# Kernel optimization log

Hardware: AMD Instinct MI355X
Metric: run time of the kernel (lower is better)

Reference implementation:

```python
import jax, jax.numpy as jnp
import numpy as np

TEMPERATURE = 0.9  # DiversityLoss temperature
EPS = 1e-6


def setup_inputs() -> dict:
    key = jax.random.key(0)
    kx, ke = jax.random.split(key)
    x = jax.random.normal(kx, (8, 4096, 128), dtype=jnp.float32)
    embed = jax.random.normal(ke, (2048, 128), dtype=jnp.float32)  # [codebook_size, dim]
    return {"x": x, "embed": embed}


def reference(x, embed):
    """EuclideanCodebook.forward (ema_update=True, eval mode: no buffer updates).

    Returns (quantize, embed_ind, diversity_loss).
    """
    shape = x.shape
    xf = x.reshape(-1, shape[-1])                       # [N, d]
    x_sq = jnp.sum(xf * xf, axis=1, keepdims=True)      # [N, 1]
    e_sq = jnp.sum(embed * embed, axis=1)[None, :]      # [1, K]
    confidence = -(x_sq - 2.0 * (xf @ embed.T) + e_sq)  # [N, K]
    embed_ind_flat = jnp.argmax(confidence, axis=-1)    # [N]
    # dequantize: gather codebook rows, restore leading shape
    quantize = jnp.take(embed, embed_ind_flat, axis=0).reshape(shape)
    embed_ind = embed_ind_flat.reshape(shape[:-1])
    # diversity loss: softmax over codes per point, mean over points, entropy-style sum
    point_probs = jax.nn.softmax(confidence / TEMPERATURE, axis=1)  # [N, K]
    class_probs = jnp.mean(point_probs, axis=0)                      # [K]
    diversity_loss = jnp.sum(class_probs * jnp.log(class_probs + EPS))
    return quantize, embed_ind, diversity_loss
```

## Files before the change

### kernel.cpp

```cpp
#include <hip/hip_runtime.h>
#include <math.h>

#define D        128
#define TM       64
#define TKC      64
#define ESTRIDE  136
#define INV_T    (1.0f / 0.9f)
#define LO_SCALE 4096.0f
#define LO_INV   (1.0f / 4096.0f)

typedef _Float16 half8 __attribute__((ext_vector_type(8)));
typedef float    f32x4 __attribute__((ext_vector_type(4)));

__global__ void prep_kernel(const float* __restrict__ embed,
                            float* __restrict__ e_sq,
                            _Float16* __restrict__ e_hi,
                            _Float16* __restrict__ e_lo,
                            float* __restrict__ classacc) {
    const int c = blockIdx.x;
    const int t = threadIdx.x;
    float v0 = embed[(size_t)c * D + t];
    float v1 = embed[(size_t)c * D + 64 + t];
    _Float16 h0 = (_Float16)v0;
    _Float16 h1 = (_Float16)v1;
    e_hi[(size_t)c * D + t]      = h0;
    e_hi[(size_t)c * D + 64 + t] = h1;
    e_lo[(size_t)c * D + t]      = (_Float16)((v0 - (float)h0) * LO_SCALE);
    e_lo[(size_t)c * D + 64 + t] = (_Float16)((v1 - (float)h1) * LO_SCALE);
    float s = v0 * v0 + v1 * v1;
    #pragma unroll
    for (int off = 32; off > 0; off >>= 1) s += __shfl_down(s, off, 64);
    if (t == 0) {
        e_sq[c] = s;
        classacc[c] = 0.0f;
    }
}

__device__ __forceinline__ void stage_e(const uint4* __restrict__ ehi_g4,
                                        const uint4* __restrict__ elo_g4,
                                        _Float16* ehi, _Float16* elo,
                                        int ch, int tid) {
    #pragma unroll
    for (int it = 0; it < 4; ++it) {
        int j   = tid + it * 256;
        int row = j >> 4;
        int c8  = j & 15;
        uint4 vh = ehi_g4[(size_t)ch * (TKC * 16) + j];
        uint4 vl = elo_g4[(size_t)ch * (TKC * 16) + j];
        *(uint4*)&ehi[row * ESTRIDE + c8 * 8] = vh;
        *(uint4*)&elo[row * ESTRIDE + c8 * 8] = vl;
    }
}

__device__ __forceinline__ void mfma_chunk(const _Float16* ehi, const _Float16* elo,
                                           const half8* ahi, const half8* alo,
                                           int col, int quad,
                                           f32x4 chh[4], f32x4 cx[4]) {
    #pragma unroll
    for (int kk = 0; kk < 4; ++kk) {
        #pragma unroll
        for (int t = 0; t < 4; ++t) {
            const int boff = (16 * t + col) * ESTRIDE + kk * 32 + quad * 8;
            half8 bhi = *(const half8*)&ehi[boff];
            half8 blo = *(const half8*)&elo[boff];
            chh[t] = __builtin_amdgcn_mfma_f32_16x16x32_f16(ahi[kk], bhi, chh[t], 0, 0, 0);
            cx[t]  = __builtin_amdgcn_mfma_f32_16x16x32_f16(ahi[kk], blo, cx[t], 0, 0, 0);
            cx[t]  = __builtin_amdgcn_mfma_f32_16x16x32_f16(alo[kk], bhi, cx[t], 0, 0, 0);
        }
    }
}

__global__ __launch_bounds__(256)
void fused_kernel(const float* __restrict__ x, const float* __restrict__ embed,
                  const _Float16* __restrict__ e_hi_g, const _Float16* __restrict__ e_lo_g,
                  const float* __restrict__ e_sq_g,
                  float* __restrict__ classacc,
                  float* __restrict__ q_out, float* __restrict__ ind_out, int K) {
    __shared__ _Float16 ehi[TKC * ESTRIDE];
    __shared__ _Float16 elo[TKC * ESTRIDE];
    __shared__ float esq_s[2048];
    __shared__ float cacc_s[2048];
    __shared__ float r_s[TM];
    __shared__ int   idx_s[TM];

    const int tid  = threadIdx.x;
    const int w    = tid >> 6;
    const int lane = tid & 63;
    const int col  = lane & 15;
    const int quad = lane >> 4;
    const int p0   = blockIdx.x * TM;
    const int pr   = p0 + 16 * w + col;

    for (int i = tid; i < K; i += 256) { esq_s[i] = e_sq_g[i]; cacc_s[i] = 0.0f; }

    half8 ahi[4], alo[4];
    #pragma unroll
    for (int kk = 0; kk < 4; ++kk) {
        const float* src = x + (size_t)pr * D + kk * 32 + quad * 8;
        #pragma unroll
        for (int j = 0; j < 8; ++j) {
            float v = src[j];
            _Float16 h = (_Float16)v;
            ahi[kk][j] = h;
            alo[kk][j] = (_Float16)((v - (float)h) * LO_SCALE);
        }
    }

    const uint4* ehi_g4 = (const uint4*)e_hi_g;
    const uint4* elo_g4 = (const uint4*)e_lo_g;
    const int nch = K / TKC;

    float lrun[4] = {0.f, 0.f, 0.f, 0.f};
    float bval[4] = {-INFINITY, -INFINITY, -INFINITY, -INFINITY};
    int   bidx[4] = {0, 0, 0, 0};

    for (int ch = 0; ch < nch; ++ch) {
        __syncthreads();
        stage_e(ehi_g4, elo_g4, ehi, elo, ch, tid);
        __syncthreads();
        f32x4 chh[4], cx[4];
        #pragma unroll
        for (int t = 0; t < 4; ++t) { chh[t] = (f32x4){0,0,0,0}; cx[t] = (f32x4){0,0,0,0}; }
        mfma_chunk(ehi, elo, ahi, alo, col, quad, chh, cx);
        #pragma unroll
        for (int t = 0; t < 4; ++t) {
            const int code = ch * TKC + 16 * t + col;
            const float esq = esq_s[code];
            #pragma unroll
            for (int r = 0; r < 4; ++r) {
                float s = 2.0f * (chh[t][r] + cx[t][r] * LO_INV) - esq;
                lrun[r] += __expf(s * INV_T);
                if (s > bval[r]) { bval[r] = s; bidx[r] = code; }
            }
        }
    }

    #pragma unroll
    for (int r = 0; r < 4; ++r) {
        float v = bval[r]; int bi = bidx[r]; float l = lrun[r];
        #pragma unroll
        for (int off = 8; off >= 1; off >>= 1) {
            float ov = __shfl_xor(v, off, 16);
            int   oi = __shfl_xor(bi, off, 16);
            float ol = __shfl_xor(l, off, 16);
            l += ol;
            if (ov > v || (ov == v && oi < bi)) { v = ov; bi = oi; }
        }
        if (col == 0) {
            int row = 16 * w + quad * 4 + r;
            r_s[row]   = 1.0f / l;
            idx_s[row] = bi;
            ind_out[p0 + row] = (float)bi;
        }
    }
    __syncthreads();

    float rrow[4];
    #pragma unroll
    for (int r = 0; r < 4; ++r) rrow[r] = r_s[16 * w + quad * 4 + r];

    for (int ch = 0; ch < nch; ++ch) {
        __syncthreads();
        stage_e(ehi_g4, elo_g4, ehi, elo, ch, tid);
        __syncthreads();
        f32x4 chh[4], cx[4];
        #pragma unroll
        for (int t = 0; t < 4; ++t) { chh[t] = (f32x4){0,0,0,0}; cx[t] = (f32x4){0,0,0,0}; }
        mfma_chunk(ehi, elo, ahi, alo, col, quad, chh, cx);
        #pragma unroll
        for (int t = 0; t < 4; ++t) {
            const int code = ch * TKC + 16 * t + col;
            const float esq = esq_s[code];
            float wsum = 0.0f;
            #pragma unroll
            for (int r = 0; r < 4; ++r) {
                float s = 2.0f * (chh[t][r] + cx[t][r] * LO_INV) - esq;
                wsum += __expf(s * INV_T) * rrow[r];
            }
            wsum += __shfl_xor(wsum, 16, 64);
            wsum += __shfl_xor(wsum, 32, 64);
            if (quad == 0) atomicAdd(&cacc_s[code], wsum);
        }
    }

    __syncthreads();
    for (int i = tid; i < K; i += 256) atomicAdd(&classacc[i], cacc_s[i]);

    const float4* emb4 = (const float4*)embed;
    float4* q4 = (float4*)q_out;
    #pragma unroll
    for (int it = 0; it < 8; ++it) {
        int j = tid + it * 256;
        int row = j >> 5, d4 = j & 31;
        q4[(size_t)(p0 + row) * 32 + d4] = emb4[(size_t)idx_s[row] * 32 + d4];
    }
}

__global__ void finalize_kernel(const float* __restrict__ classacc,
                                float* __restrict__ loss_out, int N, int K) {
    __shared__ float red[256];
    const int tid = threadIdx.x;
    float s = 0.0f;
    const float invN = 1.0f / (float)N;
    for (int i = tid; i < K; i += 256) {
        float cp = classacc[i] * invN;
        s += cp * logf(cp + 1e-6f);
    }
    red[tid] = s;
    __syncthreads();
    for (int off = 128; off > 0; off >>= 1) {
        if (tid < off) red[tid] += red[tid + off];
        __syncthreads();
    }
    if (tid == 0) loss_out[0] = red[0];
}

extern "C" void kernel_launch(void* const* d_in, const int* in_sizes, int n_in,
                              void* d_out, int out_size, void* d_ws, size_t ws_size,
                              hipStream_t stream) {
    const float* x     = (const float*)d_in[0];
    const float* embed = (const float*)d_in[1];
    const int N = in_sizes[0] / D;
    const int K = in_sizes[1] / D;

    float* out      = (float*)d_out;
    float* q_out    = out;
    float* ind_out  = out + (size_t)N * D;
    float* loss_out = ind_out + N;

    float*    e_sq = (float*)d_ws;
    float*    cacc = e_sq + K;
    _Float16* e_hi = (_Float16*)(cacc + K);
    _Float16* e_lo = e_hi + (size_t)K * D;

    prep_kernel<<<K, 64, 0, stream>>>(embed, e_sq, e_hi, e_lo, cacc);
    fused_kernel<<<N / TM, 256, 0, stream>>>(x, embed, e_hi, e_lo, e_sq,
                                             cacc, q_out, ind_out, K);
    finalize_kernel<<<1, 256, 0, stream>>>(cacc, loss_out, N, K);
}
```

Before: 225.7 us.

## Keep codebook slice in registers and split codes across blocks with partial combine

Replaces the single fused kernel with two sweeps. Each block keeps a 256-code codebook slice resident in registers and streams 64-point tiles of x through shared memory. A combine kernel merges per-slice max, argmax and sum-exp, and a separate gather kernel writes the quantized rows. This removes the repeated per-chunk codebook restaging through LDS and raises parallelism. In exchange it adds launches, intermediate global buffers, and converts x to hi/lo eight times per pass. Sizes are hardcoded to the test shape.

```diff
diff --git a/kernel.cpp b/kernel.cpp
--- a/kernel.cpp
+++ b/kernel.cpp
@@ -2,14 +2,19 @@
 #include <math.h>
 
 #define D        128
-#define TM       64
-#define TKC      64
-#define ESTRIDE  136
+#define KCODES   2048
+#define NPTS     32768
+#define AS       136
 #define INV_T    (1.0f / 0.9f)
 #define LO_SCALE 4096.0f
 #define LO_INV   (1.0f / 4096.0f)
+#define CHUNK    64
+#define NCHUNK   8
+#define PSLICES  64
+#define CSLICES  8
 
 typedef _Float16 half8 __attribute__((ext_vector_type(8)));
+typedef _Float16 half4 __attribute__((ext_vector_type(4)));
 typedef float    f32x4 __attribute__((ext_vector_type(4)));
 
 __global__ void prep_kernel(const float* __restrict__ embed,
@@ -36,164 +41,249 @@
     }
 }
 
-__device__ __forceinline__ void stage_e(const uint4* __restrict__ ehi_g4,
-                                        const uint4* __restrict__ elo_g4,
-                                        _Float16* ehi, _Float16* elo,
-                                        int ch, int tid) {
-    #pragma unroll
-    for (int it = 0; it < 4; ++it) {
-        int j   = tid + it * 256;
-        int row = j >> 4;
-        int c8  = j & 15;
-        uint4 vh = ehi_g4[(size_t)ch * (TKC * 16) + j];
-        uint4 vl = elo_g4[(size_t)ch * (TKC * 16) + j];
-        *(uint4*)&ehi[row * ESTRIDE + c8 * 8] = vh;
-        *(uint4*)&elo[row * ESTRIDE + c8 * 8] = vl;
-    }
-}
-
-__device__ __forceinline__ void mfma_chunk(const _Float16* ehi, const _Float16* elo,
-                                           const half8* ahi, const half8* alo,
-                                           int col, int quad,
-                                           f32x4 chh[4], f32x4 cx[4]) {
-    #pragma unroll
-    for (int kk = 0; kk < 4; ++kk) {
-        #pragma unroll
-        for (int t = 0; t < 4; ++t) {
-            const int boff = (16 * t + col) * ESTRIDE + kk * 32 + quad * 8;
-            half8 bhi = *(const half8*)&ehi[boff];
-            half8 blo = *(const half8*)&elo[boff];
-            chh[t] = __builtin_amdgcn_mfma_f32_16x16x32_f16(ahi[kk], bhi, chh[t], 0, 0, 0);
-            cx[t]  = __builtin_amdgcn_mfma_f32_16x16x32_f16(ahi[kk], blo, cx[t], 0, 0, 0);
-            cx[t]  = __builtin_amdgcn_mfma_f32_16x16x32_f16(alo[kk], bhi, cx[t], 0, 0, 0);
-        }
-    }
-}
-
-__global__ __launch_bounds__(256)
-void fused_kernel(const float* __restrict__ x, const float* __restrict__ embed,
-                  const _Float16* __restrict__ e_hi_g, const _Float16* __restrict__ e_lo_g,
-                  const float* __restrict__ e_sq_g,
-                  float* __restrict__ classacc,
-                  float* __restrict__ q_out, float* __restrict__ ind_out, int K) {
-    __shared__ _Float16 ehi[TKC * ESTRIDE];
-    __shared__ _Float16 elo[TKC * ESTRIDE];
-    __shared__ float esq_s[2048];
-    __shared__ float cacc_s[2048];
-    __shared__ float r_s[TM];
-    __shared__ int   idx_s[TM];
+__device__ __forceinline__ void stage_x(const float4* __restrict__ x4,
+                                        _Float16* ahi, _Float16* alo,
+                                        int pbase, int tid) {
+    #pragma unroll
+    for (int it = 0; it < 8; ++it) {
+        int j = tid + it * 256;
+        int row = j >> 5;
+        int d4 = j & 31;
+        float4 v = x4[(size_t)(pbase + row) * 32 + d4];
+        half4 h, l4;
+        h.x = (_Float16)v.x; h.y = (_Float16)v.y;
+        h.z = (_Float16)v.z; h.w = (_Float16)v.w;
+        l4.x = (_Float16)((v.x - (float)h.x) * LO_SCALE);
+        l4.y = (_Float16)((v.y - (float)h.y) * LO_SCALE);
+        l4.z = (_Float16)((v.z - (float)h.z) * LO_SCALE);
+        l4.w = (_Float16)((v.w - (float)h.w) * LO_SCALE);
+        *(half4*)&ahi[row * AS + d4 * 4] = h;
+        *(half4*)&alo[row * AS + d4 * 4] = l4;
+    }
+}
+
+__global__ __launch_bounds__(256, 2)
+void sweepA_kernel(const float* __restrict__ x,
+                   const _Float16* __restrict__ e_hi_g,
+                   const _Float16* __restrict__ e_lo_g,
+                   const float* __restrict__ e_sq_g,
+                   float* __restrict__ pm, float* __restrict__ pl,
+                   int* __restrict__ pidx) {
+    __shared__ _Float16 ahi[CHUNK * AS];
+    __shared__ _Float16 alo[CHUNK * AS];
+    __shared__ float cm[4][CHUNK];
+    __shared__ float cl[4][CHUNK];
+    __shared__ int   ci[4][CHUNK];
 
     const int tid  = threadIdx.x;
     const int w    = tid >> 6;
     const int lane = tid & 63;
     const int col  = lane & 15;
     const int quad = lane >> 4;
-    const int p0   = blockIdx.x * TM;
-    const int pr   = p0 + 16 * w + col;
-
-    for (int i = tid; i < K; i += 256) { esq_s[i] = e_sq_g[i]; cacc_s[i] = 0.0f; }
-
-    half8 ahi[4], alo[4];
-    #pragma unroll
-    for (int kk = 0; kk < 4; ++kk) {
-        const float* src = x + (size_t)pr * D + kk * 32 + quad * 8;
+    const int cslice = blockIdx.y;
+    const int pbase0 = blockIdx.x * (CHUNK * NCHUNK);
+    const int c0w = cslice * 256 + w * 64;
+
+    half8 bhi[4][4], blo[4][4];
+    float esq_r[4];
+    #pragma unroll
+    for (int ct = 0; ct < 4; ++ct) {
+        esq_r[ct] = e_sq_g[c0w + 16 * ct + col];
         #pragma unroll
-        for (int j = 0; j < 8; ++j) {
-            float v = src[j];
-            _Float16 h = (_Float16)v;
-            ahi[kk][j] = h;
-            alo[kk][j] = (_Float16)((v - (float)h) * LO_SCALE);
-        }
-    }
-
-    const uint4* ehi_g4 = (const uint4*)e_hi_g;
-    const uint4* elo_g4 = (const uint4*)e_lo_g;
-    const int nch = K / TKC;
-
-    float lrun[4] = {0.f, 0.f, 0.f, 0.f};
-    float bval[4] = {-INFINITY, -INFINITY, -INFINITY, -INFINITY};
-    int   bidx[4] = {0, 0, 0, 0};
-
-    for (int ch = 0; ch < nch; ++ch) {
-        __syncthreads();
-        stage_e(ehi_g4, elo_g4, ehi, elo, ch, tid);
-        __syncthreads();
-        f32x4 chh[4], cx[4];
+        for (int kk = 0; kk < 4; ++kk) {
+            size_t off = (size_t)(c0w + 16 * ct + col) * D + kk * 32 + quad * 8;
+            bhi[ct][kk] = *(const half8*)(e_hi_g + off);
+            blo[ct][kk] = *(const half8*)(e_lo_g + off);
+        }
+    }
+
+    const float4* x4 = (const float4*)x;
+
+    for (int chunk = 0; chunk < NCHUNK; ++chunk) {
+        const int pbase = pbase0 + chunk * CHUNK;
+        __syncthreads();
+        stage_x(x4, ahi, alo, pbase, tid);
+        __syncthreads();
+
         #pragma unroll
-        for (int t = 0; t < 4; ++t) { chh[t] = (f32x4){0,0,0,0}; cx[t] = (f32x4){0,0,0,0}; }
-        mfma_chunk(ehi, elo, ahi, alo, col, quad, chh, cx);
+        for (int p = 0; p < 4; ++p) {
+            half8 Ahi[4], Alo[4];
+            #pragma unroll
+            for (int kk = 0; kk < 4; ++kk) {
+                int off = (16 * p + col) * AS + kk * 32 + quad * 8;
+                Ahi[kk] = *(const half8*)&ahi[off];
+                Alo[kk] = *(const half8*)&alo[off];
+            }
+            f32x4 chh[4], cx[4];
+            #pragma unroll
+            for (int ct = 0; ct < 4; ++ct) { chh[ct] = (f32x4){0,0,0,0}; cx[ct] = (f32x4){0,0,0,0}; }
+            #pragma unroll
+            for (int kk = 0; kk < 4; ++kk) {
+                #pragma unroll
+                for (int ct = 0; ct < 4; ++ct) {
+                    chh[ct] = __builtin_amdgcn_mfma_f32_16x16x32_f16(Ahi[kk], bhi[ct][kk], chh[ct], 0, 0, 0);
+                    cx[ct]  = __builtin_amdgcn_mfma_f32_16x16x32_f16(Ahi[kk], blo[ct][kk], cx[ct], 0, 0, 0);
+                    cx[ct]  = __builtin_amdgcn_mfma_f32_16x16x32_f16(Alo[kk], bhi[ct][kk], cx[ct], 0, 0, 0);
+                }
+            }
+            float lp[4] = {0.f, 0.f, 0.f, 0.f};
+            float bv[4] = {-INFINITY, -INFINITY, -INFINITY, -INFINITY};
+            int   bi[4] = {0, 0, 0, 0};
+            #pragma unroll
+            for (int ct = 0; ct < 4; ++ct) {
+                int code = c0w + 16 * ct + col;
+                #pragma unroll
+                for (int r = 0; r < 4; ++r) {
+                    float s = 2.0f * (chh[ct][r] + cx[ct][r] * LO_INV) - esq_r[ct];
+                    lp[r] += __expf(s * INV_T);
+                    if (s > bv[r]) { bv[r] = s; bi[r] = code; }
+                }
+            }
+            #pragma unroll
+            for (int r = 0; r < 4; ++r) {
+                float v = bv[r]; int idx = bi[r]; float l = lp[r];
+                #pragma unroll
+                for (int off = 8; off >= 1; off >>= 1) {
+                    float ov = __shfl_xor(v, off, 16);
+                    int   oi = __shfl_xor(idx, off, 16);
+                    float ol = __shfl_xor(l, off, 16);
+                    l += ol;
+                    if (ov > v || (ov == v && oi < idx)) { v = ov; idx = oi; }
+                }
+                if (col == 0) {
+                    int row = p * 16 + quad * 4 + r;
+                    cm[w][row] = v; cl[w][row] = l; ci[w][row] = idx;
+                }
+            }
+        }
+        __syncthreads();
+        if (tid < CHUNK) {
+            float bm = cm[0][tid]; int bidx = ci[0][tid]; float l = cl[0][tid];
+            #pragma unroll
+            for (int ww = 1; ww < 4; ++ww) {
+                float v = cm[ww][tid]; int idx = ci[ww][tid];
+                l += cl[ww][tid];
+                if (v > bm) { bm = v; bidx = idx; }
+            }
+            size_t o = (size_t)cslice * NPTS + pbase + tid;
+            pm[o] = bm; pl[o] = l; pidx[o] = bidx;
+        }
+    }
+}
+
+__global__ void combine_kernel(const float* __restrict__ pm, const float* __restrict__ pl,
+                               const int* __restrict__ pidx,
+                               float* __restrict__ r_buf, int* __restrict__ idx_buf,
+                               float* __restrict__ ind_out) {
+    const int p = blockIdx.x * 256 + threadIdx.x;
+    float bm = -INFINITY; int bi = 0; float l = 0.0f;
+    #pragma unroll
+    for (int sl = 0; sl < CSLICES; ++sl) {
+        size_t o = (size_t)sl * NPTS + p;
+        float v = pm[o];
+        l += pl[o];
+        if (v > bm) { bm = v; bi = pidx[o]; }
+    }
+    r_buf[p] = 1.0f / l;
+    idx_buf[p] = bi;
+    ind_out[p] = (float)bi;
+}
+
+__global__ __launch_bounds__(256, 2)
+void sweepB_kernel(const float* __restrict__ x,
+                   const _Float16* __restrict__ e_hi_g,
+                   const _Float16* __restrict__ e_lo_g,
+                   const float* __restrict__ e_sq_g,
+                   const float* __restrict__ r_buf,
+                   float* __restrict__ classacc) {
+    __shared__ _Float16 ahi[CHUNK * AS];
+    __shared__ _Float16 alo[CHUNK * AS];
+    __shared__ float r_s[CHUNK];
+
+    const int tid  = threadIdx.x;
+    const int w    = tid >> 6;
+    const int lane = tid & 63;
+    const int col  = lane & 15;
+    const int quad = lane >> 4;
+    const int cslice = blockIdx.y;
+    const int pbase0 = blockIdx.x * (CHUNK * NCHUNK);
+    const int c0w = cslice * 256 + w * 64;
+
+    half8 bhi[4][4], blo[4][4];
+    float esq_r[4];
+    #pragma unroll
+    for (int ct = 0; ct < 4; ++ct) {
+        esq_r[ct] = e_sq_g[c0w + 16 * ct + col];
         #pragma unroll
-        for (int t = 0; t < 4; ++t) {
-            const int code = ch * TKC + 16 * t + col;
-            const float esq = esq_s[code];
-            #pragma unroll
-            for (int r = 0; r < 4; ++r) {
-                float s = 2.0f * (chh[t][r] + cx[t][r] * LO_INV) - esq;
-                lrun[r] += __expf(s * INV_T);
-                if (s > bval[r]) { bval[r] = s; bidx[r] = code; }
-            }
-        }
-    }
-
-    #pragma unroll
-    for (int r = 0; r < 4; ++r) {
-        float v = bval[r]; int bi = bidx[r]; float l = lrun[r];
+        for (int kk = 0; kk < 4; ++kk) {
+            size_t off = (size_t)(c0w + 16 * ct + col) * D + kk * 32 + quad * 8;
+            bhi[ct][kk] = *(const half8*)(e_hi_g + off);
+            blo[ct][kk] = *(const half8*)(e_lo_g + off);
+        }
+    }
+
+    const float4* x4 = (const float4*)x;
+    float csum[4] = {0.f, 0.f, 0.f, 0.f};
+
+    for (int chunk = 0; chunk < NCHUNK; ++chunk) {
+        const int pbase = pbase0 + chunk * CHUNK;
+        __syncthreads();
+        stage_x(x4, ahi, alo, pbase, tid);
+        if (tid < CHUNK) r_s[tid] = r_buf[pbase + tid];
+        __syncthreads();
+
         #pragma unroll
-        for (int off = 8; off >= 1; off >>= 1) {
-            float ov = __shfl_xor(v, off, 16);
-            int   oi = __shfl_xor(bi, off, 16);
-            float ol = __shfl_xor(l, off, 16);
-            l += ol;
-            if (ov > v || (ov == v && oi < bi)) { v = ov; bi = oi; }
-        }
-        if (col == 0) {
-            int row = 16 * w + quad * 4 + r;
-            r_s[row]   = 1.0f / l;
-            idx_s[row] = bi;
-            ind_out[p0 + row] = (float)bi;
-        }
-    }
-    __syncthreads();
-
-    float rrow[4];
-    #pragma unroll
-    for (int r = 0; r < 4; ++r) rrow[r] = r_s[16 * w + quad * 4 + r];
-
-    for (int ch = 0; ch < nch; ++ch) {
-        __syncthreads();
-        stage_e(ehi_g4, elo_g4, ehi, elo, ch, tid);
-        __syncthreads();
-        f32x4 chh[4], cx[4];
-        #pragma unroll
-        for (int t = 0; t < 4; ++t) { chh[t] = (f32x4){0,0,0,0}; cx[t] = (f32x4){0,0,0,0}; }
-        mfma_chunk(ehi, elo, ahi, alo, col, quad, chh, cx);
-        #pragma unroll
-        for (int t = 0; t < 4; ++t) {
-            const int code = ch * TKC + 16 * t + col;
-            const float esq = esq_s[code];
-            float wsum = 0.0f;
-            #pragma unroll
-            for (int r = 0; r < 4; ++r) {
-                float s = 2.0f * (chh[t][r] + cx[t][r] * LO_INV) - esq;
-                wsum += __expf(s * INV_T) * rrow[r];
-            }
-            wsum += __shfl_xor(wsum, 16, 64);
-            wsum += __shfl_xor(wsum, 32, 64);
-            if (quad == 0) atomicAdd(&cacc_s[code], wsum);
-        }
-    }
-
-    __syncthreads();
-    for (int i = tid; i < K; i += 256) atomicAdd(&classacc[i], cacc_s[i]);
-
-    const float4* emb4 = (const float4*)embed;
-    float4* q4 = (float4*)q_out;
-    #pragma unroll
-    for (int it = 0; it < 8; ++it) {
-        int j = tid + it * 256;
-        int row = j >> 5, d4 = j & 31;
-        q4[(size_t)(p0 + row) * 32 + d4] = emb4[(size_t)idx_s[row] * 32 + d4];
-    }
+        for (int p = 0; p < 4; ++p) {
+            half8 Ahi[4], Alo[4];
+            #pragma unroll
+            for (int kk = 0; kk < 4; ++kk) {
+                int off = (16 * p + col) * AS + kk * 32 + quad * 8;
+                Ahi[kk] = *(const half8*)&ahi[off];
+                Alo[kk] = *(const half8*)&alo[off];
+            }
+            f32x4 chh[4], cx[4];
+            #pragma unroll
+            for (int ct = 0; ct < 4; ++ct) { chh[ct] = (f32x4){0,0,0,0}; cx[ct] = (f32x4){0,0,0,0}; }
+            #pragma unroll
+            for (int kk = 0; kk < 4; ++kk) {
+                #pragma unroll
+                for (int ct = 0; ct < 4; ++ct) {
+                    chh[ct] = __builtin_amdgcn_mfma_f32_16x16x32_f16(Ahi[kk], bhi[ct][kk], chh[ct], 0, 0, 0);
+                    cx[ct]  = __builtin_amdgcn_mfma_f32_16x16x32_f16(Ahi[kk], blo[ct][kk], cx[ct], 0, 0, 0);
+                    cx[ct]  = __builtin_amdgcn_mfma_f32_16x16x32_f16(Alo[kk], bhi[ct][kk], cx[ct], 0, 0, 0);
+                }
+            }
+            float rr[4];
+            #pragma unroll
+            for (int r = 0; r < 4; ++r) rr[r] = r_s[p * 16 + quad * 4 + r];
+            #pragma unroll
+            for (int ct = 0; ct < 4; ++ct) {
+                #pragma unroll
+                for (int r = 0; r < 4; ++r) {
+                    float s = 2.0f * (chh[ct][r] + cx[ct][r] * LO_INV) - esq_r[ct];
+                    csum[ct] += __expf(s * INV_T) * rr[r];
+                }
+            }
+        }
+    }
+
+    #pragma unroll
+    for (int ct = 0; ct < 4; ++ct) {
+        float v = csum[ct];
+        v += __shfl_xor(v, 16, 64);
+        v += __shfl_xor(v, 32, 64);
+        if (quad == 0) atomicAdd(&classacc[c0w + 16 * ct + col], v);
+    }
+}
+
+__global__ void gather_kernel(const float* __restrict__ embed,
+                              const int* __restrict__ idx_buf,
+                              float* __restrict__ q_out) {
+    const int j = blockIdx.x * 256 + threadIdx.x;
+    const int row = j >> 5;
+    const int d4 = j & 31;
+    reinterpret_cast<float4*>(q_out)[(size_t)row * 32 + d4] =
+        reinterpret_cast<const float4*>(embed)[(size_t)idx_buf[row] * 32 + d4];
 }
 
 __global__ void finalize_kernel(const float* __restrict__ classacc,
@@ -220,21 +310,28 @@
                               hipStream_t stream) {
     const float* x     = (const float*)d_in[0];
     const float* embed = (const float*)d_in[1];
-    const int N = in_sizes[0] / D;
-    const int K = in_sizes[1] / D;
 
     float* out      = (float*)d_out;
     float* q_out    = out;
-    float* ind_out  = out + (size_t)N * D;
-    float* loss_out = ind_out + N;
-
-    float*    e_sq = (float*)d_ws;
-    float*    cacc = e_sq + K;
-    _Float16* e_hi = (_Float16*)(cacc + K);
-    _Float16* e_lo = e_hi + (size_t)K * D;
-
-    prep_kernel<<<K, 64, 0, stream>>>(embed, e_sq, e_hi, e_lo, cacc);
-    fused_kernel<<<N / TM, 256, 0, stream>>>(x, embed, e_hi, e_lo, e_sq,
-                                             cacc, q_out, ind_out, K);
-    finalize_kernel<<<1, 256, 0, stream>>>(cacc, loss_out, N, K);
-}
+    float* ind_out  = out + (size_t)NPTS * D;
+    float* loss_out = ind_out + NPTS;
+
+    float*    e_sq  = (float*)d_ws;
+    float*    cacc  = e_sq + KCODES;
+    _Float16* e_hi  = (_Float16*)(cacc + KCODES);
+    _Float16* e_lo  = e_hi + (size_t)KCODES * D;
+    float*    pm    = (float*)(e_lo + (size_t)KCODES * D);
+    float*    pl    = pm + (size_t)CSLICES * NPTS;
+    int*      pidx  = (int*)(pl + (size_t)CSLICES * NPTS);
+    float*    r_buf = (float*)(pidx + (size_t)CSLICES * NPTS);
+    int*      idx_buf = (int*)(r_buf + NPTS);
+
+    dim3 sgrid(PSLICES, CSLICES);
+
+    prep_kernel<<<KCODES, 64, 0, stream>>>(embed, e_sq, e_hi, e_lo, cacc);
+    sweepA_kernel<<<sgrid, 256, 0, stream>>>(x, e_hi, e_lo, e_sq, pm, pl, pidx);
+    combine_kernel<<<NPTS / 256, 256, 0, stream>>>(pm, pl, pidx, r_buf, idx_buf, ind_out);
+    sweepB_kernel<<<sgrid, 256, 0, stream>>>(x, e_hi, e_lo, e_sq, r_buf, cacc);
+    gather_kernel<<<NPTS * 32 / 256, 256, 0, stream>>>(embed, idx_buf, q_out);
+    finalize_kernel<<<1, 256, 0, stream>>>(cacc, loss_out, NPTS, KCODES);
+}
```

After: 225.5 us. Within noise of the previous version (-0.1%).
